# Kernel tuning notes

Hardware: AMD Instinct MI355X
Metric: run time of the kernel (lower is better)

The kernel has to match this reference:

```python
import math
import jax, jax.numpy as jnp
import numpy as np


def setup_inputs() -> dict:
    key = jax.random.key(0)
    kq, kk, kv = jax.random.split(key, 3)
    B, H, S, D = 2, 16, 2048, 64
    q = jax.random.normal(kq, (B, H, S, D), dtype=jnp.float32)
    k = jax.random.normal(kk, (B, H, S, D), dtype=jnp.float32)
    v = jax.random.normal(kv, (B, H, S, D), dtype=jnp.float32)
    return {"q": q, "k": k, "v": v}


def reference(q, k, v):
    # Retention-style linear attention with per-head exponential decay.
    # Per-head decay rate: gamma_h = 1 - 2^(-5-h); mask D[h,i,j] = gamma_h^(i-j) for i>=j else 0.
    B, H, S, Dh = q.shape
    scale = 1.0 / math.sqrt(Dh)
    h = jnp.arange(H, dtype=jnp.float32)
    s_val = jnp.log2(1.0 - jnp.exp2(-5.0 - h))  # log2(gamma_h), [H]
    idx = jnp.arange(S)
    diff = (idx[:, None] - idx[None, :]).astype(jnp.float32)  # [S, S]
    causal = idx[:, None] >= idx[None, :]
    # decay[h,i,j] = 2^((i-j) * log2(gamma_h)) on the causal region, 0 above diagonal
    decay = jnp.where(causal[None], jnp.exp2(diff[None] * s_val[:, None, None]), 0.0)  # [H,S,S]
    scores = jnp.einsum("bhsd,bhtd->bhst", q, k) * scale  # [B,H,S,S]
    out = jnp.einsum("bhst,bhtd->bhsd", scores * decay[None], v)
    return out
```

## Files before the change

### kernel.cpp

```cpp
#include <hip/hip_runtime.h>
#include <math.h>

namespace {
constexpr int kB = 2, kH = 16, kS = 2048, kD = 64, kC = 64;
constexpr int kNC = kS / kC;
constexpr int kG = 8;
constexpr int kCPG = kNC / kG;
constexpr int kBH = kB * kH;
constexpr float kScale = 0.125f;
constexpr unsigned long long kMagic = 0x9E3779B97F4A7C15ull;
}

typedef _Float16 f16;
typedef f16 f16x8 __attribute__((ext_vector_type(8)));
typedef f16 f16x4 __attribute__((ext_vector_type(4)));
typedef float f32x4 __attribute__((ext_vector_type(4)));

__device__ __forceinline__ int swz(int row, int col) {
  return row * 64 + (col ^ ((row & 7) << 3));
}

__global__ __launch_bounds__(1024, 4) void ret_fused(
    const float* __restrict__ Q, const float* __restrict__ K,
    const float* __restrict__ V, unsigned long long* __restrict__ flags,
    float* __restrict__ Lbuf, float* __restrict__ O) {
  const int blk = blockIdx.x;
  const int g   = blk >> 5;
  const int bh  = blk & 31;
  const int h   = bh & 15;
  const int t   = threadIdx.x;
  const int lane = t & 63, wv = t >> 6, r16 = lane & 15, g4 = lane >> 4;
  const int ri = wv >> 2;
  const int ch = wv & 3;
  const int erow = ri * 16 + g4 * 4;

  __shared__ f16 qs[4096];
  __shared__ f16 ks[4096];
  __shared__ f16 ktd[4096];
  __shared__ f16 vt[4096];
  __shared__ f16 ptl[4096];
  __shared__ f16 sp[4096];
  __shared__ float pt[kC + 1];

  const float log2g = log2f(1.0f - exp2f(-5.0f - (float)h));
  if (t <= kC) pt[t] = exp2f((float)t * log2g);
  const float gC64 = exp2f(64.0f * log2g);

  const size_t hbase = (size_t)bh * (kS * kD);

  float4 pfq, pfk, pfv;
  {
    const size_t cb = hbase + (size_t)(kCPG * g) * 4096;
    pfq = ((const float4*)(Q + cb))[t];
    pfk = ((const float4*)(K + cb))[t];
    pfv = ((const float4*)(V + cb))[t];
  }

  float Lr[4];
#pragma unroll
  for (int m = 0; m < 4; ++m) Lr[m] = 0.f;
  f32x4 acc[kCPG];
#pragma unroll
  for (int r = 0; r < kCPG; ++r) acc[r] = f32x4{0.f, 0.f, 0.f, 0.f};
  f16x8 aQ[kCPG][2];

#pragma unroll
  for (int r = 0; r < kCPG; ++r) {
    __syncthreads();
    {
      const int row = t >> 4, c4 = t & 15;
      *(f16x4*)&qs[swz(row, c4 * 4)] =
          f16x4{(f16)pfq.x, (f16)pfq.y, (f16)pfq.z, (f16)pfq.w};
      *(f16x4*)&ks[swz(row, c4 * 4)] =
          f16x4{(f16)pfk.x, (f16)pfk.y, (f16)pfk.z, (f16)pfk.w};
      const float w = pt[63 - row];
      ktd[swz(c4 * 4 + 0, row)] = (f16)(pfk.x * w);
      ktd[swz(c4 * 4 + 1, row)] = (f16)(pfk.y * w);
      ktd[swz(c4 * 4 + 2, row)] = (f16)(pfk.z * w);
      ktd[swz(c4 * 4 + 3, row)] = (f16)(pfk.w * w);
      vt[swz(c4 * 4 + 0, row)] = (f16)pfv.x;
      vt[swz(c4 * 4 + 1, row)] = (f16)pfv.y;
      vt[swz(c4 * 4 + 2, row)] = (f16)pfv.z;
      vt[swz(c4 * 4 + 3, row)] = (f16)pfv.w;
    }
#pragma unroll
    for (int rr = 0; rr < 4; ++rr)
      ptl[swz(erow + rr, ch * 16 + r16)] = (f16)Lr[rr];
    if (r < kCPG - 1) {
      const size_t cb = hbase + (size_t)(kCPG * g + r + 1) * 4096;
      pfq = ((const float4*)(Q + cb))[t];
      pfk = ((const float4*)(K + cb))[t];
      pfv = ((const float4*)(V + cb))[t];
    }
    __syncthreads();

    const f16x8 aQ0 = *(const f16x8*)&qs[swz(ri * 16 + r16, g4 * 8)];
    const f16x8 aQ1 = *(const f16x8*)&qs[swz(ri * 16 + r16, 32 + g4 * 8)];
    aQ[r][0] = aQ0; aQ[r][1] = aQ1;

    {
      const f16x8 b0 = *(const f16x8*)&ks[swz(ch * 16 + r16, g4 * 8)];
      const f16x8 b1 = *(const f16x8*)&ks[swz(ch * 16 + r16, 32 + g4 * 8)];
      f32x4 c = {0.f, 0.f, 0.f, 0.f};
      c = __builtin_amdgcn_mfma_f32_16x16x32_f16(aQ0, b0, c, 0, 0, 0);
      c = __builtin_amdgcn_mfma_f32_16x16x32_f16(aQ1, b1, c, 0, 0, 0);
#pragma unroll
      for (int rr = 0; rr < 4; ++rr) {
        const int i = erow + rr, j = ch * 16 + r16;
        const float w = (j <= i) ? kScale * pt[i - j] : 0.f;
        sp[swz(i, j)] = (f16)(c[rr] * w);
      }
    }
    {
      const f16x8 b0 = *(const f16x8*)&ptl[swz(ch * 16 + r16, g4 * 8)];
      const f16x8 b1 = *(const f16x8*)&ptl[swz(ch * 16 + r16, 32 + g4 * 8)];
      f32x4 c = {0.f, 0.f, 0.f, 0.f};
      c = __builtin_amdgcn_mfma_f32_16x16x32_f16(aQ0, b0, c, 0, 0, 0);
      c = __builtin_amdgcn_mfma_f32_16x16x32_f16(aQ1, b1, c, 0, 0, 0);
#pragma unroll
      for (int rr = 0; rr < 4; ++rr)
        acc[r][rr] += kScale * pt[erow + rr + 1] * c[rr];
    }
    {
      const f16x8 aV0 = *(const f16x8*)&vt[swz(ri * 16 + r16, g4 * 8)];
      const f16x8 aV1 = *(const f16x8*)&vt[swz(ri * 16 + r16, 32 + g4 * 8)];
      const f16x8 b0 = *(const f16x8*)&ktd[swz(ch * 16 + r16, g4 * 8)];
      const f16x8 b1 = *(const f16x8*)&ktd[swz(ch * 16 + r16, 32 + g4 * 8)];
      f32x4 c = {0.f, 0.f, 0.f, 0.f};
      c = __builtin_amdgcn_mfma_f32_16x16x32_f16(aV0, b0, c, 0, 0, 0);
      c = __builtin_amdgcn_mfma_f32_16x16x32_f16(aV1, b1, c, 0, 0, 0);
#pragma unroll
      for (int rr = 0; rr < 4; ++rr)
        Lr[rr] = gC64 * Lr[rr] + c[rr];
    }
    __syncthreads();
    {
      const f16x8 aS0 = *(const f16x8*)&sp[swz(ri * 16 + r16, g4 * 8)];
      const f16x8 aS1 = *(const f16x8*)&sp[swz(ri * 16 + r16, 32 + g4 * 8)];
      const f16x8 b0 = *(const f16x8*)&vt[swz(ch * 16 + r16, g4 * 8)];
      const f16x8 b1 = *(const f16x8*)&vt[swz(ch * 16 + r16, 32 + g4 * 8)];
      acc[r] = __builtin_amdgcn_mfma_f32_16x16x32_f16(aS0, b0, acc[r], 0, 0, 0);
      acc[r] = __builtin_amdgcn_mfma_f32_16x16x32_f16(aS1, b1, acc[r], 0, 0, 0);
    }
  }

  if (g < kG - 1) {
    float* Lb = Lbuf + (size_t)(bh * kG + g) * 4096;
#pragma unroll
    for (int rr = 0; rr < 4; ++rr)
      __hip_atomic_store(&Lb[(erow + rr) * 64 + ch * 16 + r16], Lr[rr],
                         __ATOMIC_RELAXED, __HIP_MEMORY_SCOPE_AGENT);
    asm volatile("s_waitcnt vmcnt(0)" ::: "memory");
  }
  __syncthreads();
  if (g < kG - 1 && t == 0)
    __hip_atomic_store(&flags[bh * kG + g], kMagic, __ATOMIC_RELAXED,
                       __HIP_MEMORY_SCOPE_AGENT);

  if (g > 0) {
    if (t < g) {
      while (__hip_atomic_load(&flags[bh * kG + t], __ATOMIC_RELAXED,
                               __HIP_MEMORY_SCOPE_AGENT) != kMagic)
        __builtin_amdgcn_s_sleep(8);
    }
    __syncthreads();
    float pin[4];
#pragma unroll
    for (int m = 0; m < 4; ++m) pin[m] = 0.f;
    for (int gp = 0; gp < g; ++gp) {
      const float w = exp2f(256.0f * (float)(g - 1 - gp) * log2g);
      const float* Lb = Lbuf + (size_t)(bh * kG + gp) * 4096;
#pragma unroll
      for (int rr = 0; rr < 4; ++rr)
        pin[rr] += w * __hip_atomic_load(&Lb[(erow + rr) * 64 + ch * 16 + r16],
                                         __ATOMIC_RELAXED,
                                         __HIP_MEMORY_SCOPE_AGENT);
    }
#pragma unroll
    for (int rr = 0; rr < 4; ++rr)
      ptl[swz(erow + rr, ch * 16 + r16)] = (f16)pin[rr];
    __syncthreads();
#pragma unroll
    for (int r = 0; r < kCPG; ++r) {
      const float gcr = exp2f(64.0f * (float)r * log2g);
      const f16x8 b0 = *(const f16x8*)&ptl[swz(ch * 16 + r16, g4 * 8)];
      const f16x8 b1 = *(const f16x8*)&ptl[swz(ch * 16 + r16, 32 + g4 * 8)];
      f32x4 c = {0.f, 0.f, 0.f, 0.f};
      c = __builtin_amdgcn_mfma_f32_16x16x32_f16(aQ[r][0], b0, c, 0, 0, 0);
      c = __builtin_amdgcn_mfma_f32_16x16x32_f16(aQ[r][1], b1, c, 0, 0, 0);
#pragma unroll
      for (int rr = 0; rr < 4; ++rr)
        acc[r][rr] += kScale * pt[erow + rr + 1] * gcr * c[rr];
    }
  }

#pragma unroll
  for (int r = 0; r < kCPG; ++r) {
    float* Ob = O + hbase + (size_t)(kCPG * g + r) * 4096;
#pragma unroll
    for (int rr = 0; rr < 4; ++rr)
      Ob[(erow + rr) * 64 + ch * 16 + r16] = acc[r][rr];
  }
}

__global__ __launch_bounds__(256) void ret_fallback(const float* __restrict__ Q,
                                                    const float* __restrict__ K,
                                                    const float* __restrict__ V,
                                                    float* __restrict__ O) {
  const int bh = blockIdx.x;
  const int h = bh % kH;
  const int t = threadIdx.x;

  __shared__ float qs[kC * 68];
  __shared__ float ks[kC * 68];
  __shared__ float vs[kC * kD];
  __shared__ float St[kD * kD];
  __shared__ float ss[kC * 65];
  __shared__ float pt[kC + 1];

  const float log2g = log2f(1.0f - exp2f(-5.0f - (float)h));
  const float gC = exp2f((float)kC * log2g);
  if (t <= kC) pt[t] = exp2f((float)t * log2g);
#pragma unroll
  for (int n = 0; n < 4; ++n) ((float4*)St)[t + 256*n] = make_float4(0.f,0.f,0.f,0.f);
  __syncthreads();

  const int i = t >> 2;
  const int e0 = (t & 3) * 16;

  for (int c = 0; c < kNC; ++c) {
    const size_t gbase = ((size_t)bh * kS + (size_t)c * kC) * kD;
#pragma unroll
    for (int n0 = 0; n0 < 4; ++n0) {
      const int n = t + 256 * n0;
      const int row = n >> 4, cc = n & 15;
      ((float4*)qs)[row * 17 + cc] = ((const float4*)(Q + gbase))[n];
      ((float4*)ks)[row * 17 + cc] = ((const float4*)(K + gbase))[n];
      ((float4*)vs)[n] = ((const float4*)(V + gbase))[n];
    }
    __syncthreads();

    float acc[16];
#pragma unroll
    for (int m = 0; m < 16; ++m) acc[m] = 0.0f;
    for (int d = 0; d < kD; ++d) {
      const float wq = qs[i * 68 + d];
      const float4* pr = (const float4*)(St + d * kD + e0);
#pragma unroll
      for (int m = 0; m < 4; ++m) {
        float4 pv = pr[m];
        acc[4*m+0]+=wq*pv.x; acc[4*m+1]+=wq*pv.y; acc[4*m+2]+=wq*pv.z; acc[4*m+3]+=wq*pv.w;
      }
    }
    const float wI = pt[i + 1];
#pragma unroll
    for (int m = 0; m < 16; ++m) acc[m] *= wI;

    {
      const int jb = t & 3;
      float part[16];
#pragma unroll
      for (int jn = 0; jn < 16; ++jn) part[jn] = 0.0f;
#pragma unroll
      for (int d4 = 0; d4 < 16; ++d4) {
        const float4 q4 = ((const float4*)qs)[i * 17 + d4];
#pragma unroll
        for (int jn = 0; jn < 16; ++jn) {
          const float4 k4 = ((const float4*)ks)[(jb + 4 * jn) * 17 + d4];
          part[jn] += q4.x*k4.x + q4.y*k4.y + q4.z*k4.z + q4.w*k4.w;
        }
      }
#pragma unroll
      for (int jn = 0; jn < 16; ++jn) {
        const int j = jb + 4 * jn;
        ss[i * 65 + j] = (j <= i) ? part[jn] * pt[i - j] : 0.0f;
      }
    }
    __syncthreads();

    {
      const int jmax = i | 15;
      for (int j = 0; j <= jmax; ++j) {
        const float w = ss[i * 65 + j];
        const float4* vr = (const float4*)(vs + j * kD + e0);
#pragma unroll
        for (int m = 0; m < 4; ++m) {
          float4 vv = vr[m];
          acc[4*m+0]+=w*vv.x; acc[4*m+1]+=w*vv.y; acc[4*m+2]+=w*vv.z; acc[4*m+3]+=w*vv.w;
        }
      }
    }

    {
      float4* obv = (float4*)(O + gbase + (size_t)i * kD + e0);
#pragma unroll
      for (int m = 0; m < 4; ++m)
        obv[m] = make_float4(kScale*acc[4*m+0], kScale*acc[4*m+1],
                             kScale*acc[4*m+2], kScale*acc[4*m+3]);
    }

    {
      float upd[16];
#pragma unroll
      for (int m = 0; m < 16; ++m) upd[m] = 0.0f;
      for (int j = 0; j < kC; ++j) {
        const float wk = pt[kC - 1 - j] * ks[j * 68 + i];
        const float4* vr = (const float4*)(vs + j * kD + e0);
#pragma unroll
        for (int m = 0; m < 4; ++m) {
          float4 vv = vr[m];
          upd[4*m+0]+=wk*vv.x; upd[4*m+1]+=wk*vv.y; upd[4*m+2]+=wk*vv.z; upd[4*m+3]+=wk*vv.w;
        }
      }
      __syncthreads();
#pragma unroll
      for (int m = 0; m < 16; ++m)
        St[i * kD + e0 + m] = gC * St[i * kD + e0 + m] + upd[m];
      __syncthreads();
    }
  }
}

extern "C" void kernel_launch(void* const* d_in, const int* in_sizes, int n_in,
                              void* d_out, int out_size, void* d_ws, size_t ws_size,
                              hipStream_t stream) {
  const float* q = (const float*)d_in[0];
  const float* k = (const float*)d_in[1];
  const float* v = (const float*)d_in[2];
  float* out = (float*)d_out;

  const size_t need = 4096 + (size_t)kBH * kG * kD * kD * sizeof(float);
  if (ws_size >= need) {
    unsigned long long* flags = (unsigned long long*)d_ws;
    float* Lbuf = (float*)((char*)d_ws + 4096);
    ret_fused<<<kBH * kG, 1024, 0, stream>>>(q, k, v, flags, Lbuf, out);
  } else {
    ret_fallback<<<kBH, 256, 0, stream>>>(q, k, v, out);
  }
}
```

Measured before the change: 21.81 us.

## Double-buffer chunk staging in LDS and prefetch two chunks ahead

Result: slower. 23.61 us (+8.2%).

```diff
diff --git a/kernel.cpp b/kernel.cpp
--- a/kernel.cpp
+++ b/kernel.cpp
@@ -34,11 +34,11 @@
   const int ch = wv & 3;
   const int erow = ri * 16 + g4 * 4;
 
-  __shared__ f16 qs[4096];
-  __shared__ f16 ks[4096];
-  __shared__ f16 ktd[4096];
-  __shared__ f16 vt[4096];
-  __shared__ f16 ptl[4096];
+  __shared__ f16 qs[2][4096];
+  __shared__ f16 ks[2][4096];
+  __shared__ f16 ktd[2][4096];
+  __shared__ f16 vt[2][4096];
+  __shared__ f16 ptl[2][4096];
   __shared__ f16 sp[4096];
   __shared__ float pt[kC + 1];
 
@@ -47,14 +47,28 @@
   const float gC64 = exp2f(64.0f * log2g);
 
   const size_t hbase = (size_t)bh * (kS * kD);
+  const int srow = t >> 4, sc4 = t & 15;
+  const float sdecay = exp2f((float)(63 - srow) * log2g);
 
   float4 pfq, pfk, pfv;
-  {
-    const size_t cb = hbase + (size_t)(kCPG * g) * 4096;
-    pfq = ((const float4*)(Q + cb))[t];
-    pfk = ((const float4*)(K + cb))[t];
-    pfv = ((const float4*)(V + cb))[t];
-  }
+#define LOADC(r_) {                                                   \
+    const size_t cb = hbase + (size_t)(kCPG * g + (r_)) * 4096;       \
+    pfq = ((const float4*)(Q + cb))[t];                               \
+    pfk = ((const float4*)(K + cb))[t];                               \
+    pfv = ((const float4*)(V + cb))[t]; }
+#define STAGE(bb) {                                                   \
+    *(f16x4*)&qs[bb][swz(srow, sc4 * 4)] =                            \
+        f16x4{(f16)pfq.x, (f16)pfq.y, (f16)pfq.z, (f16)pfq.w};        \
+    *(f16x4*)&ks[bb][swz(srow, sc4 * 4)] =                            \
+        f16x4{(f16)pfk.x, (f16)pfk.y, (f16)pfk.z, (f16)pfk.w};        \
+    ktd[bb][swz(sc4 * 4 + 0, srow)] = (f16)(pfk.x * sdecay);          \
+    ktd[bb][swz(sc4 * 4 + 1, srow)] = (f16)(pfk.y * sdecay);          \
+    ktd[bb][swz(sc4 * 4 + 2, srow)] = (f16)(pfk.z * sdecay);          \
+    ktd[bb][swz(sc4 * 4 + 3, srow)] = (f16)(pfk.w * sdecay);          \
+    vt[bb][swz(sc4 * 4 + 0, srow)] = (f16)pfv.x;                      \
+    vt[bb][swz(sc4 * 4 + 1, srow)] = (f16)pfv.y;                      \
+    vt[bb][swz(sc4 * 4 + 2, srow)] = (f16)pfv.z;                      \
+    vt[bb][swz(sc4 * 4 + 3, srow)] = (f16)pfv.w; }
 
   float Lr[4];
 #pragma unroll
@@ -64,43 +78,24 @@
   for (int r = 0; r < kCPG; ++r) acc[r] = f32x4{0.f, 0.f, 0.f, 0.f};
   f16x8 aQ[kCPG][2];
 
+  LOADC(0);
+  STAGE(0);
+#pragma unroll
+  for (int rr = 0; rr < 4; ++rr)
+    ptl[0][swz(erow + rr, ch * 16 + r16)] = (f16)0.f;
+  LOADC(1);
+  __syncthreads();
+
 #pragma unroll
   for (int r = 0; r < kCPG; ++r) {
-    __syncthreads();
-    {
-      const int row = t >> 4, c4 = t & 15;
-      *(f16x4*)&qs[swz(row, c4 * 4)] =
-          f16x4{(f16)pfq.x, (f16)pfq.y, (f16)pfq.z, (f16)pfq.w};
-      *(f16x4*)&ks[swz(row, c4 * 4)] =
-          f16x4{(f16)pfk.x, (f16)pfk.y, (f16)pfk.z, (f16)pfk.w};
-      const float w = pt[63 - row];
-      ktd[swz(c4 * 4 + 0, row)] = (f16)(pfk.x * w);
-      ktd[swz(c4 * 4 + 1, row)] = (f16)(pfk.y * w);
-      ktd[swz(c4 * 4 + 2, row)] = (f16)(pfk.z * w);
-      ktd[swz(c4 * 4 + 3, row)] = (f16)(pfk.w * w);
-      vt[swz(c4 * 4 + 0, row)] = (f16)pfv.x;
-      vt[swz(c4 * 4 + 1, row)] = (f16)pfv.y;
-      vt[swz(c4 * 4 + 2, row)] = (f16)pfv.z;
-      vt[swz(c4 * 4 + 3, row)] = (f16)pfv.w;
-    }
-#pragma unroll
-    for (int rr = 0; rr < 4; ++rr)
-      ptl[swz(erow + rr, ch * 16 + r16)] = (f16)Lr[rr];
-    if (r < kCPG - 1) {
-      const size_t cb = hbase + (size_t)(kCPG * g + r + 1) * 4096;
-      pfq = ((const float4*)(Q + cb))[t];
-      pfk = ((const float4*)(K + cb))[t];
-      pfv = ((const float4*)(V + cb))[t];
-    }
-    __syncthreads();
-
-    const f16x8 aQ0 = *(const f16x8*)&qs[swz(ri * 16 + r16, g4 * 8)];
-    const f16x8 aQ1 = *(const f16x8*)&qs[swz(ri * 16 + r16, 32 + g4 * 8)];
+    const int b = r & 1;
+    const f16x8 aQ0 = *(const f16x8*)&qs[b][swz(ri * 16 + r16, g4 * 8)];
+    const f16x8 aQ1 = *(const f16x8*)&qs[b][swz(ri * 16 + r16, 32 + g4 * 8)];
     aQ[r][0] = aQ0; aQ[r][1] = aQ1;
 
     {
-      const f16x8 b0 = *(const f16x8*)&ks[swz(ch * 16 + r16, g4 * 8)];
-      const f16x8 b1 = *(const f16x8*)&ks[swz(ch * 16 + r16, 32 + g4 * 8)];
+      const f16x8 b0 = *(const f16x8*)&ks[b][swz(ch * 16 + r16, g4 * 8)];
+      const f16x8 b1 = *(const f16x8*)&ks[b][swz(ch * 16 + r16, 32 + g4 * 8)];
       f32x4 c = {0.f, 0.f, 0.f, 0.f};
       c = __builtin_amdgcn_mfma_f32_16x16x32_f16(aQ0, b0, c, 0, 0, 0);
       c = __builtin_amdgcn_mfma_f32_16x16x32_f16(aQ1, b1, c, 0, 0, 0);
@@ -112,8 +107,8 @@
       }
     }
     {
-      const f16x8 b0 = *(const f16x8*)&ptl[swz(ch * 16 + r16, g4 * 8)];
-      const f16x8 b1 = *(const f16x8*)&ptl[swz(ch * 16 + r16, 32 + g4 * 8)];
+      const f16x8 b0 = *(const f16x8*)&ptl[b][swz(ch * 16 + r16, g4 * 8)];
+      const f16x8 b1 = *(const f16x8*)&ptl[b][swz(ch * 16 + r16, 32 + g4 * 8)];
       f32x4 c = {0.f, 0.f, 0.f, 0.f};
       c = __builtin_amdgcn_mfma_f32_16x16x32_f16(aQ0, b0, c, 0, 0, 0);
       c = __builtin_amdgcn_mfma_f32_16x16x32_f16(aQ1, b1, c, 0, 0, 0);
@@ -122,10 +117,10 @@
         acc[r][rr] += kScale * pt[erow + rr + 1] * c[rr];
     }
     {
-      const f16x8 aV0 = *(const f16x8*)&vt[swz(ri * 16 + r16, g4 * 8)];
-      const f16x8 aV1 = *(const f16x8*)&vt[swz(ri * 16 + r16, 32 + g4 * 8)];
-      const f16x8 b0 = *(const f16x8*)&ktd[swz(ch * 16 + r16, g4 * 8)];
-      const f16x8 b1 = *(const f16x8*)&ktd[swz(ch * 16 + r16, 32 + g4 * 8)];
+      const f16x8 aV0 = *(const f16x8*)&vt[b][swz(ri * 16 + r16, g4 * 8)];
+      const f16x8 aV1 = *(const f16x8*)&vt[b][swz(ri * 16 + r16, 32 + g4 * 8)];
+      const f16x8 b0 = *(const f16x8*)&ktd[b][swz(ch * 16 + r16, g4 * 8)];
+      const f16x8 b1 = *(const f16x8*)&ktd[b][swz(ch * 16 + r16, 32 + g4 * 8)];
       f32x4 c = {0.f, 0.f, 0.f, 0.f};
       c = __builtin_amdgcn_mfma_f32_16x16x32_f16(aV0, b0, c, 0, 0, 0);
       c = __builtin_amdgcn_mfma_f32_16x16x32_f16(aV1, b1, c, 0, 0, 0);
@@ -133,16 +128,26 @@
       for (int rr = 0; rr < 4; ++rr)
         Lr[rr] = gC64 * Lr[rr] + c[rr];
     }
+    if (r < kCPG - 1) {
+      STAGE(b ^ 1);
+#pragma unroll
+      for (int rr = 0; rr < 4; ++rr)
+        ptl[b ^ 1][swz(erow + rr, ch * 16 + r16)] = (f16)Lr[rr];
+      if (r < kCPG - 2) LOADC(r + 2);
+    }
     __syncthreads();
     {
       const f16x8 aS0 = *(const f16x8*)&sp[swz(ri * 16 + r16, g4 * 8)];
       const f16x8 aS1 = *(const f16x8*)&sp[swz(ri * 16 + r16, 32 + g4 * 8)];
-      const f16x8 b0 = *(const f16x8*)&vt[swz(ch * 16 + r16, g4 * 8)];
-      const f16x8 b1 = *(const f16x8*)&vt[swz(ch * 16 + r16, 32 + g4 * 8)];
+      const f16x8 b0 = *(const f16x8*)&vt[b][swz(ch * 16 + r16, g4 * 8)];
+      const f16x8 b1 = *(const f16x8*)&vt[b][swz(ch * 16 + r16, 32 + g4 * 8)];
       acc[r] = __builtin_amdgcn_mfma_f32_16x16x32_f16(aS0, b0, acc[r], 0, 0, 0);
       acc[r] = __builtin_amdgcn_mfma_f32_16x16x32_f16(aS1, b1, acc[r], 0, 0, 0);
     }
-  }
+    __syncthreads();
+  }
+#undef LOADC
+#undef STAGE
 
   if (g < kG - 1) {
     float* Lb = Lbuf + (size_t)(bh * kG + g) * 4096;
@@ -178,13 +183,13 @@
     }
 #pragma unroll
     for (int rr = 0; rr < 4; ++rr)
-      ptl[swz(erow + rr, ch * 16 + r16)] = (f16)pin[rr];
+      ptl[0][swz(erow + rr, ch * 16 + r16)] = (f16)pin[rr];
     __syncthreads();
 #pragma unroll
     for (int r = 0; r < kCPG; ++r) {
       const float gcr = exp2f(64.0f * (float)r * log2g);
-      const f16x8 b0 = *(const f16x8*)&ptl[swz(ch * 16 + r16, g4 * 8)];
-      const f16x8 b1 = *(const f16x8*)&ptl[swz(ch * 16 + r16, 32 + g4 * 8)];
+      const f16x8 b0 = *(const f16x8*)&ptl[0][swz(ch * 16 + r16, g4 * 8)];
+      const f16x8 b1 = *(const f16x8*)&ptl[0][swz(ch * 16 + r16, 32 + g4 * 8)];
       f32x4 c = {0.f, 0.f, 0.f, 0.f};
       c = __builtin_amdgcn_mfma_f32_16x16x32_f16(aQ[r][0], b0, c, 0, 0, 0);
       c = __builtin_amdgcn_mfma_f32_16x16x32_f16(aQ[r][1], b1, c, 0, 0, 0);
```
